# Kernel tuning notes

Hardware: AMD Instinct MI355X
Metric: run time of the kernel (lower is better)

## Reference

```python
import jax, jax.numpy as jnp
from jax import lax
import numpy as np

VOCAB = 50000
EMBED = 300
H = 128
NUM_CLASS = 2
B, L = 4, 512


def _lstm(x, Wih, Whh, b):
    # x: (B, L, D) -> hidden sequence (B, L, H); PyTorch gate order i,f,g,o
    Bn = x.shape[0]
    h0 = jnp.zeros((Bn, H), dtype=x.dtype)
    c0 = jnp.zeros((Bn, H), dtype=x.dtype)

    def step(carry, xt):
        h, c = carry
        g = xt @ Wih + h @ Whh + b  # (B, 4H)
        i, f, gg, o = jnp.split(g, 4, axis=-1)
        i = jax.nn.sigmoid(i)
        f = jax.nn.sigmoid(f)
        gg = jnp.tanh(gg)
        o = jax.nn.sigmoid(o)
        c = f * c + i * gg
        h = o * jnp.tanh(c)
        return (h, c), h

    _, hs = lax.scan(step, (h0, c0), jnp.swapaxes(x, 0, 1))
    return jnp.swapaxes(hs, 0, 1)


def setup_inputs() -> dict:
    key = jax.random.key(0)
    ks = jax.random.split(key, 12)
    s = lambda fan_in: 1.0 / np.sqrt(fan_in)
    inp = {
        "question_content": jax.random.randint(ks[0], (B, L), 0, VOCAB, dtype=jnp.int32),
        "answer_content": jax.random.randint(ks[1], (B, L), 0, VOCAB, dtype=jnp.int32),
        "embed_table": jax.random.normal(ks[2], (VOCAB, EMBED), dtype=jnp.float32) * 0.1,
        "W_ih": jax.random.uniform(ks[3], (EMBED, 4 * H), jnp.float32, -s(H), s(H)),
        "W_hh": jax.random.uniform(ks[4], (H, 4 * H), jnp.float32, -s(H), s(H)),
        "b_lstm": jax.random.uniform(ks[5], (4 * H,), jnp.float32, -s(H), s(H)),
        "Wa": jax.random.uniform(ks[6], (2 * H, H), jnp.float32, -s(2 * H), s(2 * H)),
        "ba": jnp.zeros((H,), jnp.float32),
        "Wq": jax.random.uniform(ks[7], (2 * H, 1), jnp.float32, -s(2 * H), s(2 * H)),
        "bq": jnp.zeros((1,), jnp.float32),
        "Wans": jax.random.uniform(ks[8], (2 * H, 1), jnp.float32, -s(2 * H), s(2 * H)),
        "bans": jnp.zeros((1,), jnp.float32),
        "Wlast": jax.random.uniform(ks[9], (2 * H, NUM_CLASS), jnp.float32, -s(2 * H), s(2 * H)),
        "blast": jnp.zeros((NUM_CLASS,), jnp.float32),
    }
    return inp


def reference(question_content, answer_content, embed_table, W_ih, W_hh, b_lstm,
              Wa, ba, Wq, bq, Wans, bans, Wlast, blast):
    q_emb = embed_table[question_content]  # (B, Lq, EMBED)
    a_emb = embed_table[answer_content]    # (B, La, EMBED)
    q_lstm = _lstm(q_emb, W_ih, W_hh, b_lstm)  # (B, Lq, H)
    a_lstm = _lstm(a_emb, W_ih, W_hh, b_lstm)  # (B, La, H)

    # A = tanh(Wa @ cat(q_expand, a_expand) + ba); split Wa to avoid the concat copy
    Wa_q, Wa_a = Wa[:H], Wa[H:]
    proj_q = q_lstm @ Wa_q              # (B, Lq, H)
    proj_a = a_lstm @ Wa_a              # (B, La, H)
    A = jnp.tanh(proj_q[:, :, None, :] + proj_a[:, None, :, :] + ba)  # (B, Lq, La, H)

    r_q = jnp.max(A, axis=1)  # max over question positions -> (B, La, H)
    r_a = jnp.max(A, axis=2)  # max over answer positions   -> (B, Lq, H)

    cat_q = jnp.concatenate([q_lstm, r_q], axis=-1)  # (B, L, 2H) (Lq == La)
    cat_a = jnp.concatenate([a_lstm, r_a], axis=-1)
    alpha_q = jax.nn.softmax(cat_q @ Wq + bq, axis=-2)    # (B, L, 1)
    alpha_a = jax.nn.softmax(cat_a @ Wans + bans, axis=-2)

    feature_q = jnp.sum(alpha_q * r_q, axis=-2)  # (B, H)
    feature_a = jnp.sum(alpha_a * r_a, axis=-2)  # (B, H)
    feature_last = jnp.concatenate([feature_q, feature_a], axis=-1)  # (B, 2H)

    score = jax.nn.log_softmax(feature_last @ Wlast + blast, axis=-1)
    predict = jnp.argmax(score, axis=-1)
    return score, predict
```

## Files before the change

### kernel.cpp

```cpp
#include <hip/hip_runtime.h>
#include <hip/hip_bf16.h>

#define EMBED 300
#define HD    128
#define LLEN  512
#define G4    512

#define OFF_LSTM 2097152
#define OFF_PROJ 2621440
#define OFF_MX   3145728

typedef _Float16 half8 __attribute__((ext_vector_type(8)));
typedef float    f32x4 __attribute__((ext_vector_type(4)));

__device__ __forceinline__ float fsig(float x) {
    return __fdividef(1.f, 1.f + __expf(-x));
}
__device__ __forceinline__ float ftanh(float x) {
    return 1.f - __fdividef(2.f, __expf(2.f * x) + 1.f);
}

__global__ __launch_bounds__(256) void k1_gemm(
    const int* __restrict__ qc, const int* __restrict__ ac,
    const float* __restrict__ emb, const float* __restrict__ wih,
    const float* __restrict__ bl, float* __restrict__ preg)
{
    __shared__ float As[32][65];
    __shared__ float Bs[32][64];
    const int m0 = blockIdx.x * 64;
    const int n0 = blockIdx.y * 64;
    const int tid = threadIdx.x;
    const int tx = tid & 15, ty = tid >> 4;
    float acc[4][4] = {};

    for (int k0 = 0; k0 < 300; k0 += 32) {
        #pragma unroll
        for (int i = 0; i < 8; ++i) {
            int e = tid + i * 256;
            int m = e >> 5, kk = e & 31;
            int row = m0 + m;
            int c = row >> 11, b = (row >> 9) & 3, t = row & 511;
            int tok = (c == 0 ? qc : ac)[b * LLEN + t];
            int k = k0 + kk;
            As[kk][m] = (k < 300) ? emb[(size_t)tok * EMBED + k] : 0.f;
        }
        #pragma unroll
        for (int i = 0; i < 8; ++i) {
            int e = tid + i * 256;
            int kk = e >> 6, n = e & 63;
            int k = k0 + kk;
            Bs[kk][n] = (k < 300) ? wih[k * G4 + n0 + n] : 0.f;
        }
        __syncthreads();
        #pragma unroll
        for (int kk = 0; kk < 32; ++kk) {
            float a[4], bv[4];
            #pragma unroll
            for (int i = 0; i < 4; ++i) a[i] = As[kk][ty * 4 + i];
            #pragma unroll
            for (int j = 0; j < 4; ++j) bv[j] = Bs[kk][tx * 4 + j];
            #pragma unroll
            for (int i = 0; i < 4; ++i)
                #pragma unroll
                for (int j = 0; j < 4; ++j)
                    acc[i][j] += a[i] * bv[j];
        }
        __syncthreads();
    }
    #pragma unroll
    for (int i = 0; i < 4; ++i) {
        int row = m0 + ty * 4 + i;
        #pragma unroll
        for (int j = 0; j < 4; ++j) {
            int n = n0 + tx * 4 + j;
            preg[(size_t)row * G4 + n] = acc[i][j] + bl[n];
        }
    }
}

__global__ __launch_bounds__(512, 1) void k2_lstm_mfma(
    const float* __restrict__ whh, const float* __restrict__ preg,
    const float* __restrict__ wa,
    float* __restrict__ lstm, float* __restrict__ proj, float* __restrict__ mx)
{
    const int seq = blockIdx.x;
    const int tid = threadIdx.x;
    const int w  = tid >> 6;
    const int l  = tid & 63;
    const int li = l & 15;
    const int g  = l >> 4;

    __shared__ __align__(16) _Float16 hist[32 * 136];

    half8 afrag[4][4];
    #pragma unroll
    for (int s = 0; s < 4; ++s) {
        const int mg = s * 128 + w * 16 + li;
        #pragma unroll
        for (int kt = 0; kt < 4; ++kt) {
            half8 v;
            #pragma unroll
            for (int e = 0; e < 8; ++e)
                v[e] = (_Float16)whh[(kt * 32 + g * 8 + e) * G4 + mg];
            afrag[kt][s] = v;
        }
    }
    const int s_side = seq >> 2;
    half8 afragW[4];
    #pragma unroll
    for (int kt = 0; kt < 4; ++kt) {
        half8 v;
        #pragma unroll
        for (int e = 0; e < 8; ++e)
            v[e] = (_Float16)wa[(s_side * 128 + kt * 32 + g * 8 + e) * 128 + (w * 16 + li)];
        afragW[kt] = v;
    }

    for (int i = tid; i < 32 * 68; i += 512) ((unsigned*)hist)[i] = 0u;

    const f32x4* pg4 = (const f32x4*)(preg + (size_t)seq * LLEN * G4);
    const int pgo = w * 4 + g;
    const int r   = li & 3;
    const int unit = w * 16 + g * 4 + r;
    const bool wlane = li < 4;
    float* outp = lstm + (size_t)seq * LLEN * HD + unit;
    float cst = 0.f;
    float pmr0 = -1e30f, pmr1 = -1e30f, pmr2 = -1e30f, pmr3 = -1e30f;

    f32x4 pgA[4], pgB[4];
    #pragma unroll
    for (int s = 0; s < 4; ++s) pgA[s] = pg4[0 * 128 + s * 32 + pgo];
    #pragma unroll
    for (int s = 0; s < 4; ++s) pgB[s] = pg4[1 * 128 + s * 32 + pgo];

    __syncthreads();

#define LSTM_STEP(T, PGV, RD, WR)                                              \
    {                                                                          \
        half8 bfrag[4];                                                        \
        _Pragma("unroll")                                                      \
        for (int kt = 0; kt < 4; ++kt)                                         \
            bfrag[kt] = *(const half8*)((RD) + kt * 32 + g * 8);               \
        f32x4 a0 = PGV[0], a1 = PGV[1], a2 = PGV[2], a3 = PGV[3];              \
        {                                                                      \
            int tp = (T) + 2; if (tp > 511) tp = 511;                          \
            _Pragma("unroll")                                                  \
            for (int s = 0; s < 4; ++s) PGV[s] = pg4[tp * 128 + s * 32 + pgo]; \
        }                                                                      \
        _Pragma("unroll")                                                      \
        for (int kt = 0; kt < 4; ++kt) {                                       \
            a0 = __builtin_amdgcn_mfma_f32_16x16x32_f16(afrag[kt][0], bfrag[kt], a0, 0, 0, 0); \
            a1 = __builtin_amdgcn_mfma_f32_16x16x32_f16(afrag[kt][1], bfrag[kt], a1, 0, 0, 0); \
            a2 = __builtin_amdgcn_mfma_f32_16x16x32_f16(afrag[kt][2], bfrag[kt], a2, 0, 0, 0); \
            a3 = __builtin_amdgcn_mfma_f32_16x16x32_f16(afrag[kt][3], bfrag[kt], a3, 0, 0, 0); \
        }                                                                      \
        float xi = (r == 0) ? a0[0] : (r == 1) ? a0[1] : (r == 2) ? a0[2] : a0[3]; \
        float xf = (r == 0) ? a1[0] : (r == 1) ? a1[1] : (r == 2) ? a1[2] : a1[3]; \
        float xg = (r == 0) ? a2[0] : (r == 1) ? a2[1] : (r == 2) ? a2[2] : a2[3]; \
        float xo = (r == 0) ? a3[0] : (r == 1) ? a3[1] : (r == 2) ? a3[2] : a3[3]; \
        float i_ = fsig(xi), f_ = fsig(xf), g_ = ftanh(xg), o_ = fsig(xo);     \
        cst = f_ * cst + i_ * g_;                                              \
        float h = o_ * ftanh(cst);                                             \
        if (wlane) {                                                           \
            outp[(size_t)(T) * HD] = h;                                        \
            (WR)[unit] = (_Float16)h;                                          \
        }                                                                      \
        asm volatile("s_waitcnt lgkmcnt(0)" ::: "memory");                     \
        __builtin_amdgcn_sched_barrier(0);                                     \
        __builtin_amdgcn_s_barrier();                                          \
        __builtin_amdgcn_sched_barrier(0);                                     \
    }

    #pragma unroll 1
    for (int tt = 0; tt < 256; ++tt) {
        const int t0 = tt * 2;
        const int slot = t0 & 31;
        _Float16* wr0 = hist + slot * 136;
        const _Float16* rd0 = hist + ((slot + 31) & 31) * 136;
        _Float16* wr1 = hist + (slot + 1) * 136;
        LSTM_STEP(t0,     pgA, rd0, wr0);
        LSTM_STEP(t0 + 1, pgB, wr0, wr1);
        if ((tt & 7) == 7) {
            const int p = (tt >> 3) & 1;
            const int tbase = t0 - 14;
            const _Float16* hb = hist + (p * 16 + li) * 136;
            half8 bb0 = *(const half8*)(hb + 0 * 32 + g * 8);
            half8 bb1 = *(const half8*)(hb + 1 * 32 + g * 8);
            half8 bb2 = *(const half8*)(hb + 2 * 32 + g * 8);
            half8 bb3 = *(const half8*)(hb + 3 * 32 + g * 8);
            f32x4 pa = {0.f, 0.f, 0.f, 0.f};
            pa = __builtin_amdgcn_mfma_f32_16x16x32_f16(afragW[0], bb0, pa, 0, 0, 0);
            pa = __builtin_amdgcn_mfma_f32_16x16x32_f16(afragW[1], bb1, pa, 0, 0, 0);
            pa = __builtin_amdgcn_mfma_f32_16x16x32_f16(afragW[2], bb2, pa, 0, 0, 0);
            pa = __builtin_amdgcn_mfma_f32_16x16x32_f16(afragW[3], bb3, pa, 0, 0, 0);
            float* pp = proj + (size_t)seq * LLEN * HD
                      + (size_t)(tbase + li) * HD + w * 16 + g * 4;
            *(f32x4*)pp = pa;
            pmr0 = fmaxf(pmr0, pa[0]);
            pmr1 = fmaxf(pmr1, pa[1]);
            pmr2 = fmaxf(pmr2, pa[2]);
            pmr3 = fmaxf(pmr3, pa[3]);
        }
    }
#undef LSTM_STEP

    #pragma unroll
    for (int m = 1; m <= 8; m <<= 1) {
        pmr0 = fmaxf(pmr0, __shfl_xor(pmr0, m, 64));
        pmr1 = fmaxf(pmr1, __shfl_xor(pmr1, m, 64));
        pmr2 = fmaxf(pmr2, __shfl_xor(pmr2, m, 64));
        pmr3 = fmaxf(pmr3, __shfl_xor(pmr3, m, 64));
    }
    if (li == 0) {
        mx[seq * HD + w * 16 + g * 4 + 0] = pmr0;
        mx[seq * HD + w * 16 + g * 4 + 1] = pmr1;
        mx[seq * HD + w * 16 + g * 4 + 2] = pmr2;
        mx[seq * HD + w * 16 + g * 4 + 3] = pmr3;
    }
}

__global__ __launch_bounds__(512) void k45a_attn(
    const float* __restrict__ lstm, const float* __restrict__ proj,
    const float* __restrict__ mx, const float* __restrict__ ba,
    const float* __restrict__ wq, const float* __restrict__ wans,
    float* __restrict__ pn, float* __restrict__ pd)
{
    const int bid = blockIdx.x;
    const int chunk = bid & 3, sb = bid >> 2;
    const int s = sb >> 2, b = sb & 3;
    const int tid = threadIdx.x;
    const int wave = tid >> 6, lane = tid & 63;

    __shared__ float nred[8][128];
    __shared__ float dred[8];

    const float* wv = (s == 0) ? wq : wans;
    const float* lb = lstm + (size_t)sb * LLEN * HD;
    const float* po = proj + (size_t)((1 - s) * 4 + b) * LLEN * HD;

    const float mb1 = mx[sb * HD + lane] + ba[lane];
    const float mb2 = mx[sb * HD + lane + 64] + ba[lane + 64];
    const float wv1a = wv[lane], wv1b = wv[lane + 64];
    const float wv2a = wv[128 + lane], wv2b = wv[192 + lane];

    float n1 = 0.f, n2 = 0.f, den = 0.f;
    #pragma unroll 4
    for (int jj = 0; jj < 16; ++jj) {
        const int j = chunk * 128 + wave + jj * 8;
        float L1 = lb[(size_t)j * HD + lane];
        float L2 = lb[(size_t)j * HD + lane + 64];
        float P1 = po[(size_t)j * HD + lane];
        float P2 = po[(size_t)j * HD + lane + 64];
        float r1 = ftanh(mb1 + P1), r2 = ftanh(mb2 + P2);
        float sc = L1 * wv1a + L2 * wv1b + r1 * wv2a + r2 * wv2b;
        #pragma unroll
        for (int o = 32; o; o >>= 1) sc += __shfl_xor(sc, o, 64);
        float e = __expf(sc);
        den += e;
        n1 += e * r1;
        n2 += e * r2;
    }
    nred[wave][lane] = n1;
    nred[wave][lane + 64] = n2;
    if (lane == 0) dred[wave] = den;
    __syncthreads();

    if (tid < 128) {
        float s8 = 0.f;
        #pragma unroll
        for (int i = 0; i < 8; ++i) s8 += nred[i][tid];
        pn[bid * 128 + tid] = s8;
    }
    if (tid == 128) {
        float dd = 0.f;
        #pragma unroll
        for (int i = 0; i < 8; ++i) dd += dred[i];
        pd[bid] = dd;
    }
}

__global__ __launch_bounds__(256) void k45b_final(
    const float* __restrict__ pn, const float* __restrict__ pd,
    const float* __restrict__ wlast, const float* __restrict__ blast,
    float* __restrict__ outp)
{
    const int b = blockIdx.x;
    const int tid = threadIdx.x;
    __shared__ float feats[2][128];
    __shared__ float cls[256];

    {
        const int ss = tid >> 7, h = tid & 127;
        const int base = (ss * 4 + b) * 4;
        float num = pn[(base + 0) * 128 + h] + pn[(base + 1) * 128 + h]
                  + pn[(base + 2) * 128 + h] + pn[(base + 3) * 128 + h];
        float dd  = pd[base + 0] + pd[base + 1] + pd[base + 2] + pd[base + 3];
        feats[ss][h] = num / dd;
    }
    __syncthreads();

    if (tid < 128) {
        float f0 = feats[0][tid], f1 = feats[1][tid];
        cls[tid]       = f0 * wlast[tid * 2 + 0] + f1 * wlast[(128 + tid) * 2 + 0];
        cls[128 + tid] = f0 * wlast[tid * 2 + 1] + f1 * wlast[(128 + tid) * 2 + 1];
    }
    __syncthreads();
    if (tid < 64) {
        float a0 = cls[tid] + cls[tid + 64];
        float a1 = cls[128 + tid] + cls[192 + tid];
        #pragma unroll
        for (int o = 32; o; o >>= 1) {
            a0 += __shfl_down(a0, o, 64);
            a1 += __shfl_down(a1, o, 64);
        }
        if (tid == 0) {
            float l0 = blast[0] + a0, l1 = blast[1] + a1;
            float mxl = fmaxf(l0, l1);
            float lse = mxl + logf(__expf(l0 - mxl) + __expf(l1 - mxl));
            outp[b * 2 + 0] = l0 - lse;
            outp[b * 2 + 1] = l1 - lse;
            outp[8 + b]     = (l1 > l0) ? 1.f : 0.f;
        }
    }
}

extern "C" void kernel_launch(void* const* d_in, const int* in_sizes, int n_in,
                              void* d_out, int out_size, void* d_ws, size_t ws_size,
                              hipStream_t stream)
{
    const int*   qc    = (const int*)d_in[0];
    const int*   ac    = (const int*)d_in[1];
    const float* emb   = (const float*)d_in[2];
    const float* wih   = (const float*)d_in[3];
    const float* whh   = (const float*)d_in[4];
    const float* bl    = (const float*)d_in[5];
    const float* wa    = (const float*)d_in[6];
    const float* ba    = (const float*)d_in[7];
    const float* wq    = (const float*)d_in[8];
    const float* wans  = (const float*)d_in[10];
    const float* wlast = (const float*)d_in[12];
    const float* blast = (const float*)d_in[13];

    float* ws   = (float*)d_ws;
    float* preg = ws;
    float* lstm = ws + OFF_LSTM;
    float* proj = ws + OFF_PROJ;
    float* mx   = ws + OFF_MX;
    float* pn   = ws;
    float* pd   = ws + 4096;

    k1_gemm<<<dim3(64, 8), 256, 0, stream>>>(qc, ac, emb, wih, bl, preg);
    k2_lstm_mfma<<<8, 512, 0, stream>>>(whh, preg, wa, lstm, proj, mx);
    k45a_attn<<<32, 512, 0, stream>>>(lstm, proj, mx, ba, wq, wans, pn, pd);
    k45b_final<<<4, 256, 0, stream>>>(pn, pd, wlast, blast, (float*)d_out);
}
```

Measured before the change: 389.9 us.

## Batch four LSTM sequences per block into the MFMA column dimension

The recurrent LSTM kernel now packs four sequences into the 16 N-columns of each 16x16 MFMA, instead of running one sequence per block with mostly idle columns. The grid drops from 8 blocks to 2, and each block keeps a separate fp16 hidden-state history per sequence in shared memory. The Wa projection and the running max are now done for four sequences per block. The per-step latency chain is unchanged, while each block does four times the projection and load work. The prefetch clamp at t=511 is removed, so the last steps read slightly past each sequence's preg rows, and those values are never used.

```diff
diff --git a/kernel.cpp b/kernel.cpp
--- a/kernel.cpp
+++ b/kernel.cpp
@@ -9,6 +9,8 @@
 #define OFF_LSTM 2097152
 #define OFF_PROJ 2621440
 #define OFF_MX   3145728
+
+#define SEQSTRIDE 4368
 
 typedef _Float16 half8 __attribute__((ext_vector_type(8)));
 typedef float    f32x4 __attribute__((ext_vector_type(4)));
@@ -83,14 +85,16 @@
     const float* __restrict__ wa,
     float* __restrict__ lstm, float* __restrict__ proj, float* __restrict__ mx)
 {
-    const int seq = blockIdx.x;
+    const int sg = blockIdx.x;
     const int tid = threadIdx.x;
     const int w  = tid >> 6;
     const int l  = tid & 63;
     const int li = l & 15;
     const int g  = l >> 4;
-
-    __shared__ __align__(16) _Float16 hist[32 * 136];
+    const int sq = li & 3;
+    const int r  = li >> 2;
+
+    __shared__ __align__(16) _Float16 hist[4 * SEQSTRIDE];
 
     half8 afrag[4][4];
     #pragma unroll
@@ -105,47 +109,49 @@
             afrag[kt][s] = v;
         }
     }
-    const int s_side = seq >> 2;
     half8 afragW[4];
     #pragma unroll
     for (int kt = 0; kt < 4; ++kt) {
         half8 v;
         #pragma unroll
         for (int e = 0; e < 8; ++e)
-            v[e] = (_Float16)wa[(s_side * 128 + kt * 32 + g * 8 + e) * 128 + (w * 16 + li)];
+            v[e] = (_Float16)wa[(sg * 128 + kt * 32 + g * 8 + e) * 128 + (w * 16 + li)];
         afragW[kt] = v;
     }
 
-    for (int i = tid; i < 32 * 68; i += 512) ((unsigned*)hist)[i] = 0u;
-
-    const f32x4* pg4 = (const f32x4*)(preg + (size_t)seq * LLEN * G4);
+    for (int i = tid; i < (4 * SEQSTRIDE) / 2; i += 512) ((unsigned*)hist)[i] = 0u;
+
+    const int seq = sg * 4 + sq;
+    const f32x4* pgl = (const f32x4*)(preg + (size_t)seq * LLEN * G4);
     const int pgo = w * 4 + g;
-    const int r   = li & 3;
     const int unit = w * 16 + g * 4 + r;
-    const bool wlane = li < 4;
     float* outp = lstm + (size_t)seq * LLEN * HD + unit;
+    _Float16* hwp = hist + sq * SEQSTRIDE + unit;
+    const _Float16* hrp = hist + sq * SEQSTRIDE + g * 8;
     float cst = 0.f;
-    float pmr0 = -1e30f, pmr1 = -1e30f, pmr2 = -1e30f, pmr3 = -1e30f;
+    f32x4 pmr[4];
+    #pragma unroll
+    for (int s = 0; s < 4; ++s) pmr[s] = (f32x4){-1e30f, -1e30f, -1e30f, -1e30f};
 
     f32x4 pgA[4], pgB[4];
     #pragma unroll
-    for (int s = 0; s < 4; ++s) pgA[s] = pg4[0 * 128 + s * 32 + pgo];
-    #pragma unroll
-    for (int s = 0; s < 4; ++s) pgB[s] = pg4[1 * 128 + s * 32 + pgo];
+    for (int s = 0; s < 4; ++s) pgA[s] = pgl[0 * 128 + s * 32 + pgo];
+    #pragma unroll
+    for (int s = 0; s < 4; ++s) pgB[s] = pgl[1 * 128 + s * 32 + pgo];
 
     __syncthreads();
 
-#define LSTM_STEP(T, PGV, RD, WR)                                              \
+#define LSTM_STEP(T, PGV, RDS, WRS)                                            \
     {                                                                          \
         half8 bfrag[4];                                                        \
         _Pragma("unroll")                                                      \
         for (int kt = 0; kt < 4; ++kt)                                         \
-            bfrag[kt] = *(const half8*)((RD) + kt * 32 + g * 8);               \
+            bfrag[kt] = *(const half8*)(hrp + (RDS) * 136 + kt * 32);          \
         f32x4 a0 = PGV[0], a1 = PGV[1], a2 = PGV[2], a3 = PGV[3];              \
         {                                                                      \
-            int tp = (T) + 2; if (tp > 511) tp = 511;                          \
             _Pragma("unroll")                                                  \
-            for (int s = 0; s < 4; ++s) PGV[s] = pg4[tp * 128 + s * 32 + pgo]; \
+            for (int s = 0; s < 4; ++s)                                        \
+                PGV[s] = pgl[((T) + 2) * 128 + s * 32 + pgo];                  \
         }                                                                      \
         _Pragma("unroll")                                                      \
         for (int kt = 0; kt < 4; ++kt) {                                       \
@@ -161,10 +167,8 @@
         float i_ = fsig(xi), f_ = fsig(xf), g_ = ftanh(xg), o_ = fsig(xo);     \
         cst = f_ * cst + i_ * g_;                                              \
         float h = o_ * ftanh(cst);                                             \
-        if (wlane) {                                                           \
-            outp[(size_t)(T) * HD] = h;                                        \
-            (WR)[unit] = (_Float16)h;                                          \
-        }                                                                      \
+        outp[(size_t)(T) * HD] = h;                                            \
+        hwp[(WRS) * 136] = (_Float16)h;                                        \
         asm volatile("s_waitcnt lgkmcnt(0)" ::: "memory");                     \
         __builtin_amdgcn_sched_barrier(0);                                     \
         __builtin_amdgcn_s_barrier();                                          \
@@ -174,48 +178,45 @@
     #pragma unroll 1
     for (int tt = 0; tt < 256; ++tt) {
         const int t0 = tt * 2;
-        const int slot = t0 & 31;
-        _Float16* wr0 = hist + slot * 136;
-        const _Float16* rd0 = hist + ((slot + 31) & 31) * 136;
-        _Float16* wr1 = hist + (slot + 1) * 136;
-        LSTM_STEP(t0,     pgA, rd0, wr0);
-        LSTM_STEP(t0 + 1, pgB, wr0, wr1);
+        const int s0 = t0 & 31;
+        LSTM_STEP(t0,     pgA, (s0 + 31) & 31, s0);
+        LSTM_STEP(t0 + 1, pgB, s0, s0 + 1);
         if ((tt & 7) == 7) {
             const int p = (tt >> 3) & 1;
             const int tbase = t0 - 14;
-            const _Float16* hb = hist + (p * 16 + li) * 136;
-            half8 bb0 = *(const half8*)(hb + 0 * 32 + g * 8);
-            half8 bb1 = *(const half8*)(hb + 1 * 32 + g * 8);
-            half8 bb2 = *(const half8*)(hb + 2 * 32 + g * 8);
-            half8 bb3 = *(const half8*)(hb + 3 * 32 + g * 8);
-            f32x4 pa = {0.f, 0.f, 0.f, 0.f};
-            pa = __builtin_amdgcn_mfma_f32_16x16x32_f16(afragW[0], bb0, pa, 0, 0, 0);
-            pa = __builtin_amdgcn_mfma_f32_16x16x32_f16(afragW[1], bb1, pa, 0, 0, 0);
-            pa = __builtin_amdgcn_mfma_f32_16x16x32_f16(afragW[2], bb2, pa, 0, 0, 0);
-            pa = __builtin_amdgcn_mfma_f32_16x16x32_f16(afragW[3], bb3, pa, 0, 0, 0);
-            float* pp = proj + (size_t)seq * LLEN * HD
-                      + (size_t)(tbase + li) * HD + w * 16 + g * 4;
-            *(f32x4*)pp = pa;
-            pmr0 = fmaxf(pmr0, pa[0]);
-            pmr1 = fmaxf(pmr1, pa[1]);
-            pmr2 = fmaxf(pmr2, pa[2]);
-            pmr3 = fmaxf(pmr3, pa[3]);
+            #pragma unroll
+            for (int s2 = 0; s2 < 4; ++s2) {
+                const _Float16* hb2 = hist + s2 * SEQSTRIDE + g * 8 + (p * 16 + li) * 136;
+                half8 bb0 = *(const half8*)(hb2 + 0 * 32);
+                half8 bb1 = *(const half8*)(hb2 + 1 * 32);
+                half8 bb2 = *(const half8*)(hb2 + 2 * 32);
+                half8 bb3 = *(const half8*)(hb2 + 3 * 32);
+                f32x4 pa = {0.f, 0.f, 0.f, 0.f};
+                pa = __builtin_amdgcn_mfma_f32_16x16x32_f16(afragW[0], bb0, pa, 0, 0, 0);
+                pa = __builtin_amdgcn_mfma_f32_16x16x32_f16(afragW[1], bb1, pa, 0, 0, 0);
+                pa = __builtin_amdgcn_mfma_f32_16x16x32_f16(afragW[2], bb2, pa, 0, 0, 0);
+                pa = __builtin_amdgcn_mfma_f32_16x16x32_f16(afragW[3], bb3, pa, 0, 0, 0);
+                float* pp = proj + (size_t)(sg * 4 + s2) * LLEN * HD
+                          + (size_t)(tbase + li) * HD + w * 16 + g * 4;
+                *(f32x4*)pp = pa;
+                #pragma unroll
+                for (int e = 0; e < 4; ++e) pmr[s2][e] = fmaxf(pmr[s2][e], pa[e]);
+            }
         }
     }
 #undef LSTM_STEP
 
     #pragma unroll
-    for (int m = 1; m <= 8; m <<= 1) {
-        pmr0 = fmaxf(pmr0, __shfl_xor(pmr0, m, 64));
-        pmr1 = fmaxf(pmr1, __shfl_xor(pmr1, m, 64));
-        pmr2 = fmaxf(pmr2, __shfl_xor(pmr2, m, 64));
-        pmr3 = fmaxf(pmr3, __shfl_xor(pmr3, m, 64));
-    }
-    if (li == 0) {
-        mx[seq * HD + w * 16 + g * 4 + 0] = pmr0;
-        mx[seq * HD + w * 16 + g * 4 + 1] = pmr1;
-        mx[seq * HD + w * 16 + g * 4 + 2] = pmr2;
-        mx[seq * HD + w * 16 + g * 4 + 3] = pmr3;
+    for (int s2 = 0; s2 < 4; ++s2) {
+        #pragma unroll
+        for (int e = 0; e < 4; ++e) {
+            float v = pmr[s2][e];
+            v = fmaxf(v, __shfl_xor(v, 1, 64));
+            v = fmaxf(v, __shfl_xor(v, 2, 64));
+            v = fmaxf(v, __shfl_xor(v, 4, 64));
+            v = fmaxf(v, __shfl_xor(v, 8, 64));
+            if (li == 0) mx[(sg * 4 + s2) * HD + w * 16 + g * 4 + e] = v;
+        }
     }
 }
 
@@ -350,7 +351,7 @@
     float* pd   = ws + 4096;
 
     k1_gemm<<<dim3(64, 8), 256, 0, stream>>>(qc, ac, emb, wih, bl, preg);
-    k2_lstm_mfma<<<8, 512, 0, stream>>>(whh, preg, wa, lstm, proj, mx);
+    k2_lstm_mfma<<<2, 512, 0, stream>>>(whh, preg, wa, lstm, proj, mx);
     k45a_attn<<<32, 512, 0, stream>>>(lstm, proj, mx, ba, wq, wans, pn, pd);
     k45b_final<<<4, 256, 0, stream>>>(pn, pd, wlast, blast, (float*)d_out);
 }
```

New measurement: 543.6 us. +39.4%, slower.

## Rewrite embedding-input GEMM with fp16 MFMA and register-resident weights

Applied to the files above, without the earlier changes.

The input-projection GEMM (embedding gather times W_ih) moves from an fp32 shared-memory SIMT tiling to fp16 MFMA. Each wave keeps its 32-column slice of W_ih in registers as A-fragments and streams gathered embedding rows straight from global memory, with the bias fused into the store. The grid changes to match the new tiling. The LSTM step macro now addresses hist by slot index rather than by pointer, a small addressing change. This trades fp32 precision in the input projection for fp16 and removes LDS staging, but W_ih is reloaded into registers by every block.

```diff
diff --git a/kernel.cpp b/kernel.cpp
--- a/kernel.cpp
+++ b/kernel.cpp
@@ -25,56 +25,65 @@
     const float* __restrict__ emb, const float* __restrict__ wih,
     const float* __restrict__ bl, float* __restrict__ preg)
 {
-    __shared__ float As[32][65];
-    __shared__ float Bs[32][64];
-    const int m0 = blockIdx.x * 64;
-    const int n0 = blockIdx.y * 64;
+    const int bx = blockIdx.x;
+    const int by = blockIdx.y;
     const int tid = threadIdx.x;
-    const int tx = tid & 15, ty = tid >> 4;
-    float acc[4][4] = {};
-
-    for (int k0 = 0; k0 < 300; k0 += 32) {
-        #pragma unroll
-        for (int i = 0; i < 8; ++i) {
-            int e = tid + i * 256;
-            int m = e >> 5, kk = e & 31;
-            int row = m0 + m;
-            int c = row >> 11, b = (row >> 9) & 3, t = row & 511;
-            int tok = (c == 0 ? qc : ac)[b * LLEN + t];
-            int k = k0 + kk;
-            As[kk][m] = (k < 300) ? emb[(size_t)tok * EMBED + k] : 0.f;
-        }
-        #pragma unroll
-        for (int i = 0; i < 8; ++i) {
-            int e = tid + i * 256;
-            int kk = e >> 6, n = e & 63;
-            int k = k0 + kk;
-            Bs[kk][n] = (k < 300) ? wih[k * G4 + n0 + n] : 0.f;
-        }
-        __syncthreads();
-        #pragma unroll
-        for (int kk = 0; kk < 32; ++kk) {
-            float a[4], bv[4];
+    const int w = tid >> 6;
+    const int l = tid & 63;
+    const int li = l & 15, g = l >> 4;
+    const int j0 = bx * 128 + w * 32;
+
+    half8 afragK[2][10];
+    #pragma unroll
+    for (int js = 0; js < 2; ++js) {
+        #pragma unroll
+        for (int kt = 0; kt < 10; ++kt) {
+            half8 v;
             #pragma unroll
-            for (int i = 0; i < 4; ++i) a[i] = As[kk][ty * 4 + i];
-            #pragma unroll
-            for (int j = 0; j < 4; ++j) bv[j] = Bs[kk][tx * 4 + j];
-            #pragma unroll
-            for (int i = 0; i < 4; ++i)
+            for (int e = 0; e < 8; ++e) {
+                int k = kt * 32 + g * 8 + e;
+                v[e] = (k < 300) ? (_Float16)wih[k * G4 + j0 + js * 16 + li]
+                                 : (_Float16)0.f;
+            }
+            afragK[js][kt] = v;
+        }
+    }
+    const int jc0 = j0 + g * 4, jc1 = j0 + 16 + g * 4;
+    const f32x4 bias0 = *(const f32x4*)(bl + jc0);
+    const f32x4 bias1 = *(const f32x4*)(bl + jc1);
+
+    #pragma unroll 1
+    for (int ns = 0; ns < 2; ++ns) {
+        const int row = by * 32 + ns * 16 + li;
+        const int c = row >> 11, b = (row >> 9) & 3, t = row & 511;
+        const int tok = (c == 0 ? qc : ac)[b * LLEN + t];
+        const float* er = emb + (size_t)tok * EMBED;
+        f32x4 acc0 = {0.f, 0.f, 0.f, 0.f}, acc1 = {0.f, 0.f, 0.f, 0.f};
+        #pragma unroll
+        for (int kt = 0; kt < 10; ++kt) {
+            const int kbase = kt * 32 + g * 8;
+            half8 bv;
+            if (kt < 9) {
+                float4 u0 = *(const float4*)(er + kbase);
+                float4 u1 = *(const float4*)(er + kbase + 4);
+                bv[0] = (_Float16)u0.x; bv[1] = (_Float16)u0.y;
+                bv[2] = (_Float16)u0.z; bv[3] = (_Float16)u0.w;
+                bv[4] = (_Float16)u1.x; bv[5] = (_Float16)u1.y;
+                bv[6] = (_Float16)u1.z; bv[7] = (_Float16)u1.w;
+            } else {
                 #pragma unroll
-                for (int j = 0; j < 4; ++j)
-                    acc[i][j] += a[i] * bv[j];
-        }
-        __syncthreads();
-    }
-    #pragma unroll
-    for (int i = 0; i < 4; ++i) {
-        int row = m0 + ty * 4 + i;
-        #pragma unroll
-        for (int j = 0; j < 4; ++j) {
-            int n = n0 + tx * 4 + j;
-            preg[(size_t)row * G4 + n] = acc[i][j] + bl[n];
-        }
+                for (int e = 0; e < 8; ++e) {
+                    int k = kbase + e;
+                    bv[e] = (k < 300) ? (_Float16)er[k] : (_Float16)0.f;
+                }
+            }
+            acc0 = __builtin_amdgcn_mfma_f32_16x16x32_f16(afragK[0][kt], bv, acc0, 0, 0, 0);
+            acc1 = __builtin_amdgcn_mfma_f32_16x16x32_f16(afragK[1][kt], bv, acc1, 0, 0, 0);
+        }
+        acc0 += bias0;
+        acc1 += bias1;
+        *(f32x4*)(preg + (size_t)row * G4 + jc0) = acc0;
+        *(f32x4*)(preg + (size_t)row * G4 + jc1) = acc1;
     }
 }
 
@@ -135,12 +144,12 @@
 
     __syncthreads();
 
-#define LSTM_STEP(T, PGV, RD, WR)                                              \
+#define LSTM_STEP(T, PGV, RDS, WRS)                                            \
     {                                                                          \
         half8 bfrag[4];                                                        \
         _Pragma("unroll")                                                      \
         for (int kt = 0; kt < 4; ++kt)                                         \
-            bfrag[kt] = *(const half8*)((RD) + kt * 32 + g * 8);               \
+            bfrag[kt] = *(const half8*)(hist + (RDS) * 136 + kt * 32 + g * 8); \
         f32x4 a0 = PGV[0], a1 = PGV[1], a2 = PGV[2], a3 = PGV[3];              \
         {                                                                      \
             int tp = (T) + 2; if (tp > 511) tp = 511;                          \
@@ -163,7 +172,7 @@
         float h = o_ * ftanh(cst);                                             \
         if (wlane) {                                                           \
             outp[(size_t)(T) * HD] = h;                                        \
-            (WR)[unit] = (_Float16)h;                                          \
+            hist[(WRS) * 136 + unit] = (_Float16)h;                            \
         }                                                                      \
         asm volatile("s_waitcnt lgkmcnt(0)" ::: "memory");                     \
         __builtin_amdgcn_sched_barrier(0);                                     \
@@ -175,11 +184,8 @@
     for (int tt = 0; tt < 256; ++tt) {
         const int t0 = tt * 2;
         const int slot = t0 & 31;
-        _Float16* wr0 = hist + slot * 136;
-        const _Float16* rd0 = hist + ((slot + 31) & 31) * 136;
-        _Float16* wr1 = hist + (slot + 1) * 136;
-        LSTM_STEP(t0,     pgA, rd0, wr0);
-        LSTM_STEP(t0 + 1, pgB, wr0, wr1);
+        LSTM_STEP(t0,     pgA, (slot + 31) & 31, slot);
+        LSTM_STEP(t0 + 1, pgB, slot, slot + 1);
         if ((tt & 7) == 7) {
             const int p = (tt >> 3) & 1;
             const int tbase = t0 - 14;
@@ -349,7 +355,7 @@
     float* pn   = ws;
     float* pd   = ws + 4096;
 
-    k1_gemm<<<dim3(64, 8), 256, 0, stream>>>(qc, ac, emb, wih, bl, preg);
+    k1_gemm<<<dim3(4, 128), 256, 0, stream>>>(qc, ac, emb, wih, bl, preg);
     k2_lstm_mfma<<<8, 512, 0, stream>>>(whh, preg, wa, lstm, proj, mx);
     k45a_attn<<<32, 512, 0, stream>>>(lstm, proj, mx, ba, wq, wans, pn, pd);
     k45b_final<<<4, 256, 0, stream>>>(pn, pd, wlast, blast, (float*)d_out);
```

Result: faster. 377.3 us (-3.2%).
